# Kernel optimization log

Measured on AMD Instinct MI355X. Metric: run time of the kernel, lower is better.

Reference implementation:

```python
import jax, jax.numpy as jnp
import numpy as np

N, B, D_IN, D_MID, D_OUT = 2048, 64, 768, 512, 128


def setup_inputs() -> dict:
    key = jax.random.key(0)
    ks = jax.random.split(key, 6)
    x = jax.random.normal(ks[0], (N, B, D_IN), dtype=jnp.float32)
    W1 = jax.random.normal(ks[1], (D_IN, D_MID), dtype=jnp.float32) * 0.02
    b1 = jax.random.normal(ks[2], (D_MID,), dtype=jnp.float32) * 0.02
    W2 = jax.random.normal(ks[3], (D_MID, D_OUT), dtype=jnp.float32) * 0.02
    b2 = jax.random.normal(ks[4], (D_OUT,), dtype=jnp.float32) * 0.02
    # per-sample segment lengths in [1, N//2] so segments are non-empty and in-range
    batch_list = jax.random.randint(ks[5], (B,), 1, N // 2, dtype=jnp.int32)
    return {"x": x, "W1": W1, "b1": b1, "W2": W2, "b2": b2,
            "batch_list": batch_list, "batch_size": B}


def reference(x, W1, b1, W2, b2, batch_list, batch_size):
    # x.reshape(-1, batch_size, 768).transpose(0, 1) -> (B, N, 768)
    xb = x.reshape(-1, batch_size, D_IN).transpose(1, 0, 2)
    h = jax.nn.relu(jnp.einsum('bnd,dm->bnm', xb, W1) + b1)
    x0 = jnp.einsum('bnm,mo->bno', h, W2) + b2  # (B, N, D_OUT)

    n = x0.shape[1]
    # torch code: batch_list.insert(0, 0); segment i = rows [L[i], L[i]+L[i+1]) of x_0[i]
    # i.e. start_i = (0 if i == 0 else batch_list[i-1]), len_i = batch_list[i]
    starts = jnp.concatenate([jnp.zeros((1,), jnp.int32), batch_list[:-1]])
    lens = batch_list
    j = jnp.arange(n, dtype=jnp.int32)  # (N,)
    mask = (j[None, :] >= starts[:, None]) & (j[None, :] < (starts + lens)[:, None])  # (B, N)
    neg = jnp.asarray(-jnp.inf, x0.dtype)
    x1 = jnp.where(mask[:, :, None], x0, neg).max(axis=1)  # (B, D_OUT)
    x1_probs = jnp.argmax(jax.nn.softmax(x1, axis=-1), axis=-1)
    return (x1, x1_probs)
```

## Files before the change

kernel.cpp:

```cpp
#include <hip/hip_runtime.h>
#include <math.h>

#define N_TOK 2048
#define BATCH 64
#define DIN   768
#define DMID  512
#define DOUT  128
#define TILE_N 32
#define KC    128

__device__ __forceinline__ void atomicMaxFloat(float* addr, float val) {
    if (val >= 0.0f) atomicMax((int*)addr, __float_as_int(val));
    else             atomicMin((unsigned int*)addr, __float_as_uint(val));
}

__global__ void init_kernel(float* __restrict__ x1) {
    int i = blockIdx.x * blockDim.x + threadIdx.x;
    if (i < BATCH * DOUT) x1[i] = -INFINITY;
}

__global__ __launch_bounds__(256) void fused_kernel(
    const float* __restrict__ x,
    const float* __restrict__ W1,
    const float* __restrict__ b1,
    const float* __restrict__ W2,
    const float* __restrict__ b2,
    const int*   __restrict__ batch_list,
    float* __restrict__ x1)
{
    const int b    = blockIdx.y;
    const int row0 = blockIdx.x * TILE_N;

    const int start = (b == 0) ? 0 : batch_list[b - 1];
    const int len   = batch_list[b];
    const int end   = start + len;
    if (row0 >= end || row0 + TILE_N <= start) return;

    __shared__ float xs[TILE_N][KC];
    __shared__ float hs[TILE_N][DMID];

    const int tid = threadIdx.x;

    const int tr = tid >> 6;
    const int tc = tid & 63;

    float acc[8][8];
    #pragma unroll
    for (int r = 0; r < 8; ++r)
        #pragma unroll
        for (int c = 0; c < 8; ++c) acc[r][c] = 0.0f;

    for (int kc = 0; kc < DIN; kc += KC) {
        __syncthreads();
        for (int i = tid; i < TILE_N * (KC / 4); i += 256) {
            const int r  = i / (KC / 4);
            const int kq = i % (KC / 4);
            const float4 v = *(const float4*)&x[((size_t)(row0 + r) * BATCH + b) * DIN + kc + kq * 4];
            *(float4*)&xs[r][kq * 4] = v;
        }
        __syncthreads();

        for (int k = 0; k < KC; ++k) {
            const float4 w0 = *(const float4*)&W1[(size_t)(kc + k) * DMID + tc * 8];
            const float4 w1 = *(const float4*)&W1[(size_t)(kc + k) * DMID + tc * 8 + 4];
            float wv[8] = {w0.x, w0.y, w0.z, w0.w, w1.x, w1.y, w1.z, w1.w};
            float xv[8];
            #pragma unroll
            for (int r = 0; r < 8; ++r) xv[r] = xs[tr * 8 + r][k];
            #pragma unroll
            for (int r = 0; r < 8; ++r)
                #pragma unroll
                for (int c = 0; c < 8; ++c)
                    acc[r][c] = fmaf(xv[r], wv[c], acc[r][c]);
        }
    }

    {
        const float4 bb0 = *(const float4*)&b1[tc * 8];
        const float4 bb1 = *(const float4*)&b1[tc * 8 + 4];
        const float bv[8] = {bb0.x, bb0.y, bb0.z, bb0.w, bb1.x, bb1.y, bb1.z, bb1.w};
        #pragma unroll
        for (int r = 0; r < 8; ++r)
            #pragma unroll
            for (int c = 0; c < 8; ++c)
                hs[tr * 8 + r][tc * 8 + c] = fmaxf(acc[r][c] + bv[c], 0.0f);
    }
    __syncthreads();

    const int tr2 = tid >> 5;
    const int tc2 = tid & 31;

    float acc2[4][4];
    #pragma unroll
    for (int r = 0; r < 4; ++r)
        #pragma unroll
        for (int c = 0; c < 4; ++c) acc2[r][c] = 0.0f;

    for (int k = 0; k < DMID; ++k) {
        const float4 w = *(const float4*)&W2[(size_t)k * DOUT + tc2 * 4];
        float hv[4];
        #pragma unroll
        for (int r = 0; r < 4; ++r) hv[r] = hs[tr2 * 4 + r][k];
        #pragma unroll
        for (int r = 0; r < 4; ++r) {
            acc2[r][0] = fmaf(hv[r], w.x, acc2[r][0]);
            acc2[r][1] = fmaf(hv[r], w.y, acc2[r][1]);
            acc2[r][2] = fmaf(hv[r], w.z, acc2[r][2]);
            acc2[r][3] = fmaf(hv[r], w.w, acc2[r][3]);
        }
    }

    const float4 bb = *(const float4*)&b2[tc2 * 4];
    const float bv2[4] = {bb.x, bb.y, bb.z, bb.w};
    float cmax[4] = {-INFINITY, -INFINITY, -INFINITY, -INFINITY};
    #pragma unroll
    for (int r = 0; r < 4; ++r) {
        const int row = row0 + tr2 * 4 + r;
        const bool in = (row >= start) && (row < end);
        #pragma unroll
        for (int c = 0; c < 4; ++c) {
            const float v = acc2[r][c] + bv2[c];
            if (in) cmax[c] = fmaxf(cmax[c], v);
        }
    }

    float (*red)[DOUT] = (float(*)[DOUT])xs;
    #pragma unroll
    for (int c = 0; c < 4; ++c) red[tr2][tc2 * 4 + c] = cmax[c];
    __syncthreads();

    if (tid < DOUT) {
        float m = red[0][tid];
        #pragma unroll
        for (int r = 1; r < 8; ++r) m = fmaxf(m, red[r][tid]);
        atomicMaxFloat(&x1[b * DOUT + tid], m);
    }
}

__global__ void argmax_kernel(const float* __restrict__ x1, float* __restrict__ probs) {
    int b = blockIdx.x * blockDim.x + threadIdx.x;
    if (b >= BATCH) return;
    const float* row = x1 + b * DOUT;
    float best = row[0];
    int bi = 0;
    for (int c = 1; c < DOUT; ++c) {
        float v = row[c];
        if (v > best) { best = v; bi = c; }
    }
    probs[b] = (float)bi;
}

extern "C" void kernel_launch(void* const* d_in, const int* in_sizes, int n_in,
                              void* d_out, int out_size, void* d_ws, size_t ws_size,
                              hipStream_t stream) {
    const float* x          = (const float*)d_in[0];
    const float* W1         = (const float*)d_in[1];
    const float* b1         = (const float*)d_in[2];
    const float* W2         = (const float*)d_in[3];
    const float* b2         = (const float*)d_in[4];
    const int*   batch_list = (const int*)d_in[5];

    float* x1    = (float*)d_out;
    float* probs = x1 + BATCH * DOUT;

    init_kernel<<<(BATCH * DOUT + 255) / 256, 256, 0, stream>>>(x1);

    dim3 grid(N_TOK / TILE_N, BATCH);
    fused_kernel<<<grid, 256, 0, stream>>>(x, W1, b1, W2, b2, batch_list, x1);

    argmax_kernel<<<1, 64, 0, stream>>>(x1, probs);
}
```

Before: 1.135 ms.

## Chunk hidden dimension to interleave both GEMMs and shrink shared memory

The fused MLP now walks the 512-wide hidden dimension in chunks of 128. For each chunk it computes that slice of the first GEMM with ReLU, then immediately accumulates its contribution to the second GEMM. This shrinks the hidden-activation shared buffer from the full width to one chunk, and together with a 64-row tile, a smaller K step and a launch-bounds occupancy hint it aims to fit more blocks per CU. In exchange, each block reloads its x tile once per hidden chunk, and the per-thread register tile narrows to 8x4, which lowers FMA work per LDS read.

```diff
diff --git a/kernel.cpp b/kernel.cpp
--- a/kernel.cpp
+++ b/kernel.cpp
@@ -6,8 +6,9 @@
 #define DIN   768
 #define DMID  512
 #define DOUT  128
-#define TILE_N 32
-#define KC    128
+#define TILE_N 64
+#define KC    64
+#define MC    128
 
 __device__ __forceinline__ void atomicMaxFloat(float* addr, float val) {
     if (val >= 0.0f) atomicMax((int*)addr, __float_as_int(val));
@@ -19,7 +20,7 @@
     if (i < BATCH * DOUT) x1[i] = -INFINITY;
 }
 
-__global__ __launch_bounds__(256) void fused_kernel(
+__global__ __launch_bounds__(256, 3) void fused_kernel(
     const float* __restrict__ x,
     const float* __restrict__ W1,
     const float* __restrict__ b1,
@@ -37,85 +38,93 @@
     if (row0 >= end || row0 + TILE_N <= start) return;
 
     __shared__ float xs[TILE_N][KC];
-    __shared__ float hs[TILE_N][DMID];
+    __shared__ float hs[TILE_N][MC];
 
     const int tid = threadIdx.x;
+    const int tr  = tid >> 5;
+    const int tc  = tid & 31;
 
-    const int tr = tid >> 6;
-    const int tc = tid & 63;
-
-    float acc[8][8];
+    float acc2[8][4];
     #pragma unroll
     for (int r = 0; r < 8; ++r)
         #pragma unroll
-        for (int c = 0; c < 8; ++c) acc[r][c] = 0.0f;
+        for (int c = 0; c < 4; ++c) acc2[r][c] = 0.0f;
 
-    for (int kc = 0; kc < DIN; kc += KC) {
-        __syncthreads();
-        for (int i = tid; i < TILE_N * (KC / 4); i += 256) {
-            const int r  = i / (KC / 4);
-            const int kq = i % (KC / 4);
-            const float4 v = *(const float4*)&x[((size_t)(row0 + r) * BATCH + b) * DIN + kc + kq * 4];
-            *(float4*)&xs[r][kq * 4] = v;
+    for (int mc = 0; mc < DMID; mc += MC) {
+        float acc1[8][4];
+        #pragma unroll
+        for (int r = 0; r < 8; ++r)
+            #pragma unroll
+            for (int c = 0; c < 4; ++c) acc1[r][c] = 0.0f;
+
+        const float* W1c = W1 + mc + tc * 4;
+
+        for (int kc = 0; kc < DIN; kc += KC) {
+            __syncthreads();
+            #pragma unroll
+            for (int j = 0; j < 4; ++j) {
+                const int i  = tid + j * 256;
+                const int r  = i >> 4;
+                const int kq = i & 15;
+                *(float4*)&xs[r][kq * 4] =
+                    *(const float4*)&x[((size_t)(row0 + r) * BATCH + b) * DIN + kc + kq * 4];
+            }
+            __syncthreads();
+
+            #pragma unroll 4
+            for (int k = 0; k < KC; ++k) {
+                const float4 w = *(const float4*)&W1c[(size_t)(kc + k) * DMID];
+                float xv[8];
+                #pragma unroll
+                for (int r = 0; r < 8; ++r) xv[r] = xs[tr * 8 + r][k];
+                #pragma unroll
+                for (int r = 0; r < 8; ++r) {
+                    acc1[r][0] = fmaf(xv[r], w.x, acc1[r][0]);
+                    acc1[r][1] = fmaf(xv[r], w.y, acc1[r][1]);
+                    acc1[r][2] = fmaf(xv[r], w.z, acc1[r][2]);
+                    acc1[r][3] = fmaf(xv[r], w.w, acc1[r][3]);
+                }
+            }
+        }
+
+        {
+            const float4 bb = *(const float4*)&b1[mc + tc * 4];
+            const float bv[4] = {bb.x, bb.y, bb.z, bb.w};
+            #pragma unroll
+            for (int r = 0; r < 8; ++r) {
+                float4 hv;
+                hv.x = fmaxf(acc1[r][0] + bv[0], 0.0f);
+                hv.y = fmaxf(acc1[r][1] + bv[1], 0.0f);
+                hv.z = fmaxf(acc1[r][2] + bv[2], 0.0f);
+                hv.w = fmaxf(acc1[r][3] + bv[3], 0.0f);
+                *(float4*)&hs[tr * 8 + r][tc * 4] = hv;
+            }
         }
         __syncthreads();
 
-        for (int k = 0; k < KC; ++k) {
-            const float4 w0 = *(const float4*)&W1[(size_t)(kc + k) * DMID + tc * 8];
-            const float4 w1 = *(const float4*)&W1[(size_t)(kc + k) * DMID + tc * 8 + 4];
-            float wv[8] = {w0.x, w0.y, w0.z, w0.w, w1.x, w1.y, w1.z, w1.w};
-            float xv[8];
+        const float* W2c = W2 + (size_t)mc * DOUT + tc * 4;
+        #pragma unroll 4
+        for (int kk = 0; kk < MC; ++kk) {
+            const float4 w = *(const float4*)&W2c[(size_t)kk * DOUT];
+            float hv[8];
             #pragma unroll
-            for (int r = 0; r < 8; ++r) xv[r] = xs[tr * 8 + r][k];
+            for (int r = 0; r < 8; ++r) hv[r] = hs[tr * 8 + r][kk];
             #pragma unroll
-            for (int r = 0; r < 8; ++r)
-                #pragma unroll
-                for (int c = 0; c < 8; ++c)
-                    acc[r][c] = fmaf(xv[r], wv[c], acc[r][c]);
+            for (int r = 0; r < 8; ++r) {
+                acc2[r][0] = fmaf(hv[r], w.x, acc2[r][0]);
+                acc2[r][1] = fmaf(hv[r], w.y, acc2[r][1]);
+                acc2[r][2] = fmaf(hv[r], w.z, acc2[r][2]);
+                acc2[r][3] = fmaf(hv[r], w.w, acc2[r][3]);
+            }
         }
     }
 
-    {
-        const float4 bb0 = *(const float4*)&b1[tc * 8];
-        const float4 bb1 = *(const float4*)&b1[tc * 8 + 4];
-        const float bv[8] = {bb0.x, bb0.y, bb0.z, bb0.w, bb1.x, bb1.y, bb1.z, bb1.w};
-        #pragma unroll
-        for (int r = 0; r < 8; ++r)
-            #pragma unroll
-            for (int c = 0; c < 8; ++c)
-                hs[tr * 8 + r][tc * 8 + c] = fmaxf(acc[r][c] + bv[c], 0.0f);
-    }
-    __syncthreads();
-
-    const int tr2 = tid >> 5;
-    const int tc2 = tid & 31;
-
-    float acc2[4][4];
-    #pragma unroll
-    for (int r = 0; r < 4; ++r)
-        #pragma unroll
-        for (int c = 0; c < 4; ++c) acc2[r][c] = 0.0f;
-
-    for (int k = 0; k < DMID; ++k) {
-        const float4 w = *(const float4*)&W2[(size_t)k * DOUT + tc2 * 4];
-        float hv[4];
-        #pragma unroll
-        for (int r = 0; r < 4; ++r) hv[r] = hs[tr2 * 4 + r][k];
-        #pragma unroll
-        for (int r = 0; r < 4; ++r) {
-            acc2[r][0] = fmaf(hv[r], w.x, acc2[r][0]);
-            acc2[r][1] = fmaf(hv[r], w.y, acc2[r][1]);
-            acc2[r][2] = fmaf(hv[r], w.z, acc2[r][2]);
-            acc2[r][3] = fmaf(hv[r], w.w, acc2[r][3]);
-        }
-    }
-
-    const float4 bb = *(const float4*)&b2[tc2 * 4];
-    const float bv2[4] = {bb.x, bb.y, bb.z, bb.w};
+    const float4 bb2 = *(const float4*)&b2[tc * 4];
+    const float bv2[4] = {bb2.x, bb2.y, bb2.z, bb2.w};
     float cmax[4] = {-INFINITY, -INFINITY, -INFINITY, -INFINITY};
     #pragma unroll
-    for (int r = 0; r < 4; ++r) {
-        const int row = row0 + tr2 * 4 + r;
+    for (int r = 0; r < 8; ++r) {
+        const int row = row0 + tr * 8 + r;
         const bool in = (row >= start) && (row < end);
         #pragma unroll
         for (int c = 0; c < 4; ++c) {
@@ -126,7 +135,7 @@
 
     float (*red)[DOUT] = (float(*)[DOUT])xs;
     #pragma unroll
-    for (int c = 0; c < 4; ++c) red[tr2][tc2 * 4 + c] = cmax[c];
+    for (int c = 0; c < 4; ++c) red[tr][tc * 4 + c] = cmax[c];
     __syncthreads();
 
     if (tid < DOUT) {
```

New measurement: 1.343 ms. +18.4%, slower.
